# Optimization experiments

Hardware: AMD Instinct MI355X
Metric: run time of the kernel (lower is better)

## Reference

```python
import jax, jax.numpy as jnp
import numpy as np

K = 12          # nsample_k
EPS = 1e-5      # BatchNorm eps


def _init_w(key, shape, fan_in):
    bound = 1.0 / np.sqrt(fan_in)
    return jax.random.uniform(key, shape, jnp.float32, -bound, bound)


def setup_inputs() -> dict:
    key = jax.random.key(0)
    ks = jax.random.split(key, 8)
    B, N = 4, 4096
    p = jax.random.normal(ks[0], (B, N, 3), jnp.float32)
    return {
        "p": p,
        # Conv1d(k=1) weights [out_ch, in_ch]
        "w1": _init_w(ks[1], (18, 36), 36),
        "g1": jnp.ones((18,), jnp.float32), "b1": jnp.zeros((18,), jnp.float32),
        "w2": _init_w(ks[2], (9, 18), 18),
        "g2": jnp.ones((9,), jnp.float32), "b2": jnp.zeros((9,), jnp.float32),
        "w3": _init_w(ks[3], (3, 9), 9),
        "g3": jnp.ones((3,), jnp.float32), "b3": jnp.zeros((3,), jnp.float32),
        "wr": _init_w(ks[4], (1, 3), 3),
        "br": _init_w(ks[5], (1,), 3),
    }


def _bn(x, g, b):
    # BatchNorm1d in training mode over [B, C, L]: stats over (batch, length)
    mu = jnp.mean(x, axis=(0, 2), keepdims=True)
    var = jnp.var(x, axis=(0, 2), keepdims=True)
    return g[None, :, None] * (x - mu) * jax.lax.rsqrt(var + EPS) + b[None, :, None]


def reference(p, w1, g1, b1, w2, g2, b2, w3, g3, b3, wr, br):
    B, N, _ = p.shape
    pf = p.reshape(-1, 3)                                   # [M, 3]
    # KNN over the whole flattened cloud (matches knnquery with a single offset)
    sq = jnp.sum(pf * pf, axis=1)
    d2 = sq[:, None] + sq[None, :] - 2.0 * (pf @ pf.T)       # [M, M]
    _, idx = jax.lax.top_k(-d2, K)                           # K nearest incl. self
    nidx = idx[:, 1:]                                        # drop self -> [M, K-1]
    npos = pf[nidx]                                          # [M, K-1, 3]
    # p_ij = [p_i ; |p_i - p_j|]  -> [M, K, 3] -> [M, K*3]
    pij = jnp.concatenate([pf[:, None, :], jnp.abs(pf[:, None, :] - npos)], axis=1)
    x = pij.reshape(B, N, K * 3).transpose(0, 2, 1)          # [B, 36, N]
    # pointwise MLP: 36 -> 18 -> 9 -> 3, each Conv1x1 + BN + ReLU
    h = jax.nn.relu(_bn(jnp.einsum('oi,bil->bol', w1, x), g1, b1))
    h = jax.nn.relu(_bn(jnp.einsum('oi,bil->bol', w2, h), g2, b2))
    h = jax.nn.relu(_bn(jnp.einsum('oi,bil->bol', w3, h), g3, b3))
    h = h.transpose(0, 2, 1)                                 # [B, N, 3]
    out = h @ wr.T + br                                      # [B, N, 1]
    # F.softmax with no dim on a 3-D tensor -> dim=0 (torch legacy behavior)
    out = jax.nn.softmax(out, axis=0)
    return out.reshape(-1, 1)                                # [B*N, 1]
```

## Files before the change

### kernel.cpp

```cpp
#include <hip/hip_runtime.h>
#include <math.h>

#define NTOT 16384
#define NPT  4096
#define KNN  12
#define NCH  16
#define CHS  (NTOT/NCH)
#define NSMP 128
#define K4   4
#define CAP  32
#define EPSBN 1e-5

#define D_STAT 0
#define D_COEF 60
#define D_Y1   120
#define D_Y2   (D_Y1 + NTOT*18)
#define D_Y3   (D_Y2 + NTOT*9)
#define D_END  (D_Y3 + NTOT*3)

__device__ __forceinline__ float sq_np(float x, float y, float z) {
  return __fadd_rn(__fadd_rn(__fmul_rn(x, x), __fmul_rn(y, y)), __fmul_rn(z, z));
}
__device__ __forceinline__ float d2_np(float sqq, float qx, float qy, float qz,
                                       float sqc, float cx, float cy, float cz) {
  float dot = __fadd_rn(__fadd_rn(__fmul_rn(qx, cx), __fmul_rn(qy, cy)), __fmul_rn(qz, cz));
  return __fsub_rn(__fadd_rn(sqq, sqc), __fmul_rn(2.0f, dot));
}

__global__ __launch_bounds__(256) void k_seed(const float* __restrict__ p,
                                              float* __restrict__ seedd) {
  __shared__ float4 sc[NSMP];
  const int scid = blockIdx.x & (NCH - 1);
  const int qb   = blockIdx.x >> 4;
  const int base = scid * CHS;
  if (threadIdx.x < NSMP) {
    int t = threadIdx.x;
    float x = p[3*(base+t)+0], y = p[3*(base+t)+1], z = p[3*(base+t)+2];
    sc[t] = make_float4(x, y, z, sq_np(x, y, z));
  }
  __syncthreads();
  const int q = qb*256 + (int)threadIdx.x;
  const float qx = p[3*q+0], qy = p[3*q+1], qz = p[3*q+2];
  const float sqq = sq_np(qx, qy, qz);

  float bd[K4];
  #pragma unroll
  for (int k = 0; k < K4; ++k) bd[k] = 3.4e38f;

  for (int j = 0; j < NSMP; ++j) {
    float4 c = sc[j];
    float d2 = d2_np(sqq, qx, qy, qz, c.w, c.x, c.y, c.z);
    if (d2 < bd[K4-1]) {
      #pragma unroll
      for (int k = K4-1; k >= 1; --k) {
        bool m1 = d2 < bd[k-1];
        bool m2 = d2 < bd[k];
        bd[k] = m1 ? bd[k-1] : (m2 ? d2 : bd[k]);
      }
      if (d2 < bd[0]) bd[0] = d2;
    }
  }
  const long o = ((long)q*NCH + scid)*K4;
  #pragma unroll
  for (int k = 0; k < K4; ++k) seedd[o+k] = bd[k];
}

__global__ __launch_bounds__(256) void k_thr(const float* __restrict__ seedd,
                                             float* __restrict__ thr) {
  const int q = blockIdx.x*256 + (int)threadIdx.x;
  float v[NCH*K4];
  #pragma unroll
  for (int i = 0; i < NCH*K4; ++i) v[i] = seedd[(long)q*NCH*K4 + i];
  int sel = 0; float t = 3.4e38f;
  #pragma unroll
  for (int r = 0; r < KNN; ++r) {
    if (sel < KNN) {
      float m = v[0];
      #pragma unroll
      for (int i = 1; i < NCH*K4; ++i) m = fminf(m, v[i]);
      int ce = 0;
      #pragma unroll
      for (int i = 0; i < NCH*K4; ++i) {
        bool e = (v[i] == m);
        ce += e ? 1 : 0;
        v[i] = e ? 3.4e38f : v[i];
      }
      sel += ce; t = m;
    }
  }
  thr[q] = t;
}

__global__ __launch_bounds__(256) void k_main(const float* __restrict__ p,
                                              const float* __restrict__ thr,
                                              unsigned* __restrict__ gcnt,
                                              float* __restrict__ d2f,
                                              unsigned short* __restrict__ gidx) {
  __shared__ float4 mc[CHS];
  const int c  = blockIdx.x & (NCH - 1);
  const int qb = blockIdx.x >> 4;
  const int base = c * CHS;
  for (int t = threadIdx.x; t < CHS; t += 256) {
    float x = p[3*(base+t)+0], y = p[3*(base+t)+1], z = p[3*(base+t)+2];
    mc[t] = make_float4(x, y, z, sq_np(x, y, z));
  }
  __syncthreads();
  const int q = qb*256 + (int)threadIdx.x;
  const float qx = p[3*q+0], qy = p[3*q+1], qz = p[3*q+2];
  const float sqq = sq_np(qx, qy, qz);
  const float tq  = thr[q];

  const long ob = ((long)q*NCH + c)*CAP;
  int cnt = 0;
  for (int j = 0; j < CHS; ++j) {
    float4 cd = mc[j];
    float d2 = d2_np(sqq, qx, qy, qz, cd.w, cd.x, cd.y, cd.z);
    if (d2 <= tq && cnt < CAP) {
      d2f [ob + cnt] = d2;
      gidx[ob + cnt] = (unsigned short)j;
      cnt++;
    }
  }
  gcnt[q*NCH + c] = (unsigned)cnt;
}

__global__ __launch_bounds__(64) void k_l1(const float* __restrict__ p,
                                           const unsigned* __restrict__ gcnt,
                                           const float* __restrict__ d2f,
                                           const unsigned short* __restrict__ gidx,
                                           const float* __restrict__ w1,
                                           double* __restrict__ y1,
                                           double* __restrict__ stat) {
  __shared__ float w1s[18*36];
  for (int t = threadIdx.x; t < 18*36; t += 64) w1s[t] = w1[t];
  __syncthreads();
  const int q = blockIdx.x*64 + (int)threadIdx.x;
  const double dqx = (double)p[3*q+0], dqy = (double)p[3*q+1], dqz = (double)p[3*q+2];

  float bd[KNN]; int bi[KNN];
  #pragma unroll
  for (int k = 0; k < KNN; ++k) { bd[k] = 3.4e38f; bi[k] = 0x7fffffff; }

  for (int c = 0; c < NCH; ++c) {
    int n = (int)gcnt[q*NCH + c]; n = n < CAP ? n : CAP;
    const long ob = ((long)q*NCH + c)*CAP;
    const int gb = c*CHS;
    for (int t = 0; t < n; ++t) {
      float d2 = d2f[ob + t];
      int  idx = gb + (int)gidx[ob + t];
      if (d2 < bd[KNN-1]) {
        #pragma unroll
        for (int k = KNN-1; k >= 1; --k) {
          bool m1 = d2 < bd[k-1];
          bool m2 = d2 < bd[k];
          float nv = m1 ? bd[k-1] : (m2 ? d2  : bd[k]);
          int   ni = m1 ? bi[k-1] : (m2 ? idx : bi[k]);
          bd[k] = nv; bi[k] = ni;
        }
        if (d2 < bd[0]) { bd[0] = d2; bi[0] = idx; }
      }
    }
  }

  double f[36];
  f[0] = dqx; f[1] = dqy; f[2] = dqz;
  #pragma unroll
  for (int r = 0; r < KNN-1; ++r) {
    int j = bi[r+1];
    j = (j < NTOT) ? j : q;
    f[3 + r*3 + 0] = fabs(dqx - (double)p[3*j+0]);
    f[3 + r*3 + 1] = fabs(dqy - (double)p[3*j+1]);
    f[3 + r*3 + 2] = fabs(dqz - (double)p[3*j+2]);
  }

  double v[18];
  #pragma unroll
  for (int o = 0; o < 18; ++o) {
    double s = 0.0;
    #pragma unroll
    for (int i = 0; i < 36; ++i) s += (double)w1s[o*36+i]*f[i];
    v[o] = s;
    y1[(long)q*18 + o] = s;
  }
  #pragma unroll
  for (int o = 0; o < 18; ++o) {
    double s = v[o], ss = v[o]*v[o];
    #pragma unroll
    for (int off = 32; off > 0; off >>= 1) { s += __shfl_down(s, off); ss += __shfl_down(ss, off); }
    if (threadIdx.x == 0) { atomicAdd(&stat[o], s); atomicAdd(&stat[18+o], ss); }
  }
}

__global__ void k_stats(const double* __restrict__ stat, const float* __restrict__ g,
                        const float* __restrict__ bb, double* __restrict__ coef,
                        int C, int sumoff) {
  int c = threadIdx.x;
  if (c < C) {
    const double inv = 1.0/16384.0;
    double mu   = stat[sumoff + c]*inv;
    double va   = stat[sumoff + C + c]*inv - mu*mu;
    double rstd = 1.0/sqrt(va + EPSBN);
    double a    = (double)g[c]*rstd;
    coef[c]     = a;
    coef[C + c] = (double)bb[c] - mu*a;
  }
}

__global__ __launch_bounds__(256) void k_l2(const double* __restrict__ y1,
                                            const float* __restrict__ w2,
                                            const double* __restrict__ coef,
                                            double* __restrict__ y2,
                                            double* __restrict__ stat) {
  const int q = blockIdx.x*256 + (int)threadIdx.x;
  double h[18];
  #pragma unroll
  for (int i = 0; i < 18; ++i) {
    double t = y1[(long)q*18 + i]*coef[i] + coef[18+i];
    h[i] = t > 0.0 ? t : 0.0;
  }
  #pragma unroll
  for (int o = 0; o < 9; ++o) {
    double s = 0.0;
    #pragma unroll
    for (int i = 0; i < 18; ++i) s += (double)w2[o*18+i]*h[i];
    y2[(long)q*9 + o] = s;
    double r1 = s, r2 = s*s;
    #pragma unroll
    for (int off = 32; off > 0; off >>= 1) { r1 += __shfl_down(r1, off); r2 += __shfl_down(r2, off); }
    if ((threadIdx.x & 63) == 0) { atomicAdd(&stat[36+o], r1); atomicAdd(&stat[45+o], r2); }
  }
}

__global__ __launch_bounds__(256) void k_l3(const double* __restrict__ y2,
                                            const float* __restrict__ w3,
                                            const double* __restrict__ coef,
                                            double* __restrict__ y3,
                                            double* __restrict__ stat) {
  const int q = blockIdx.x*256 + (int)threadIdx.x;
  double h[9];
  #pragma unroll
  for (int i = 0; i < 9; ++i) {
    double t = y2[(long)q*9 + i]*coef[i] + coef[9+i];
    h[i] = t > 0.0 ? t : 0.0;
  }
  #pragma unroll
  for (int o = 0; o < 3; ++o) {
    double s = 0.0;
    #pragma unroll
    for (int i = 0; i < 9; ++i) s += (double)w3[o*9+i]*h[i];
    y3[(long)q*3 + o] = s;
    double r1 = s, r2 = s*s;
    #pragma unroll
    for (int off = 32; off > 0; off >>= 1) { r1 += __shfl_down(r1, off); r2 += __shfl_down(r2, off); }
    if ((threadIdx.x & 63) == 0) { atomicAdd(&stat[54+o], r1); atomicAdd(&stat[57+o], r2); }
  }
}

__global__ __launch_bounds__(256) void k_out(const double* __restrict__ y3,
                                             const double* __restrict__ coef3,
                                             const float* __restrict__ wr,
                                             const float* __restrict__ br,
                                             float* __restrict__ out) {
  const int n = blockIdx.x*256 + (int)threadIdx.x;
  if (n >= NPT) return;
  double l[4];
  #pragma unroll
  for (int b = 0; b < 4; ++b) {
    long q = (long)b*NPT + n;
    double h0 = y3[q*3+0]*coef3[0] + coef3[3]; h0 = h0 > 0.0 ? h0 : 0.0;
    double h1 = y3[q*3+1]*coef3[1] + coef3[4]; h1 = h1 > 0.0 ? h1 : 0.0;
    double h2 = y3[q*3+2]*coef3[2] + coef3[5]; h2 = h2 > 0.0 ? h2 : 0.0;
    l[b] = h0*(double)wr[0] + h1*(double)wr[1] + h2*(double)wr[2] + (double)br[0];
  }
  double m = fmax(fmax(l[0], l[1]), fmax(l[2], l[3]));
  double e0 = exp(l[0]-m), e1 = exp(l[1]-m), e2 = exp(l[2]-m), e3 = exp(l[3]-m);
  double inv = 1.0/(e0+e1+e2+e3);
  out[0*NPT+n] = (float)(e0*inv);
  out[1*NPT+n] = (float)(e1*inv);
  out[2*NPT+n] = (float)(e2*inv);
  out[3*NPT+n] = (float)(e3*inv);
}

extern "C" void kernel_launch(void* const* d_in, const int* in_sizes, int n_in,
                              void* d_out, int out_size, void* d_ws, size_t ws_size,
                              hipStream_t stream) {
  const float* p  = (const float*)d_in[0];
  const float* w1 = (const float*)d_in[1];
  const float* g1 = (const float*)d_in[2];
  const float* b1 = (const float*)d_in[3];
  const float* w2 = (const float*)d_in[4];
  const float* g2 = (const float*)d_in[5];
  const float* b2 = (const float*)d_in[6];
  const float* w3 = (const float*)d_in[7];
  const float* g3 = (const float*)d_in[8];
  const float* b3 = (const float*)d_in[9];
  const float* wr = (const float*)d_in[10];
  const float* br = (const float*)d_in[11];

  double* wd   = (double*)d_ws;
  double* stat = wd + D_STAT;
  double* coef = wd + D_COEF;
  double* y1   = wd + D_Y1;
  double* y2   = wd + D_Y2;
  double* y3   = wd + D_Y3;
  float*  fb    = (float*)(wd + D_END);
  float*  seedd = fb;
  float*  thr   = seedd + (long)NTOT*NCH*K4;
  unsigned* gcnt = (unsigned*)(thr + NTOT);
  float*  d2f   = (float*)(gcnt + NTOT*NCH);
  unsigned short* gidx = (unsigned short*)(d2f + (long)NTOT*NCH*CAP);

  hipMemsetAsync(stat, 0, 60*sizeof(double), stream);

  hipLaunchKernelGGL(k_seed, dim3((NTOT/256)*NCH), dim3(256), 0, stream, p, seedd);
  hipLaunchKernelGGL(k_thr,  dim3(NTOT/256), dim3(256), 0, stream, seedd, thr);
  hipLaunchKernelGGL(k_main, dim3((NTOT/256)*NCH), dim3(256), 0, stream, p, thr, gcnt, d2f, gidx);
  hipLaunchKernelGGL(k_l1,   dim3(NTOT/64), dim3(64), 0, stream, p, gcnt, d2f, gidx, w1, y1, stat);
  hipLaunchKernelGGL(k_stats, dim3(1), dim3(32), 0, stream, stat, g1, b1, coef, 18, 0);
  hipLaunchKernelGGL(k_l2,   dim3(NTOT/256), dim3(256), 0, stream, y1, w2, coef, y2, stat);
  hipLaunchKernelGGL(k_stats, dim3(1), dim3(32), 0, stream, stat, g2, b2, coef+36, 9, 36);
  hipLaunchKernelGGL(k_l3,   dim3(NTOT/256), dim3(256), 0, stream, y2, w3, coef+36, y3, stat);
  hipLaunchKernelGGL(k_stats, dim3(1), dim3(32), 0, stream, stat, g3, b3, coef+54, 3, 54);
  hipLaunchKernelGGL(k_out,  dim3(NPT/256), dim3(256), 0, stream, y3, coef+54, wr, br, (float*)d_out);
}
```

Measured before the change: 439.8 us.

## Split KNN selection into a 16-lane cooperative kernel separate from layer-1 features

The fused per-point top-K insertion sort over all 16 chunk candidate lists is replaced by a separate selection kernel. In it, 16 lanes per query each scan their own chunk list and a shuffle-xor argmin picks the global minimum 12 times. A second kernel then builds features from the stored neighbour indices and computes layer 1 with 256-thread blocks. This spreads the serial selection loop across lanes to raise parallelism, at the cost of an extra launch and repeated rescans of each candidate list.

```diff
diff --git a/kernel.cpp b/kernel.cpp
--- a/kernel.cpp
+++ b/kernel.cpp
@@ -124,50 +124,62 @@
   gcnt[q*NCH + c] = (unsigned)cnt;
 }
 
-__global__ __launch_bounds__(64) void k_l1(const float* __restrict__ p,
-                                           const unsigned* __restrict__ gcnt,
-                                           const float* __restrict__ d2f,
-                                           const unsigned short* __restrict__ gidx,
-                                           const float* __restrict__ w1,
-                                           double* __restrict__ y1,
-                                           double* __restrict__ stat) {
+__global__ __launch_bounds__(256) void k_sel(const unsigned* __restrict__ gcnt,
+                                             const float* __restrict__ d2f,
+                                             const unsigned short* __restrict__ gidx,
+                                             int* __restrict__ nbr) {
+  const int grp  = (int)threadIdx.x >> 4;
+  const int lane = (int)threadIdx.x & 15;
+  const int q    = blockIdx.x*16 + grp;
+  const int slot = q*NCH + lane;
+  int n = (int)gcnt[slot]; n = n < CAP ? n : CAP;
+  const long ob = (long)slot*CAP;
+  unsigned consumed = 0;
+
+  #pragma unroll
+  for (int r = 0; r < KNN; ++r) {
+    float mind = 3.4e38f; int tmin = -1;
+    for (int t = 0; t < n; ++t) {
+      float d = d2f[ob + t];
+      bool ok = (((consumed >> t) & 1u) == 0u) && (d < mind);
+      mind = ok ? d : mind;
+      tmin = ok ? t : tmin;
+    }
+    unsigned long long key = 0xFFFFFFFFFFFFFFFFull;
+    if (tmin >= 0) {
+      unsigned u = __float_as_uint(mind);
+      u = (u & 0x80000000u) ? ~u : (u | 0x80000000u);
+      unsigned gi = (unsigned)(lane*CHS) + (unsigned)gidx[ob + tmin];
+      key = ((unsigned long long)u << 32) | gi;
+    }
+    unsigned long long kmin = key;
+    #pragma unroll
+    for (int m = 1; m < 16; m <<= 1) {
+      unsigned long long o = __shfl_xor(kmin, m);
+      kmin = (o < kmin) ? o : kmin;
+    }
+    if (key == kmin && tmin >= 0) consumed |= (1u << tmin);
+    if (lane == 0 && r > 0)
+      nbr[q*(KNN-1) + (r-1)] = (int)(unsigned)(kmin & 0xFFFFFFFFull);
+  }
+}
+
+__global__ __launch_bounds__(256) void k_feat(const float* __restrict__ p,
+                                              const int* __restrict__ nbr,
+                                              const float* __restrict__ w1,
+                                              double* __restrict__ y1,
+                                              double* __restrict__ stat) {
   __shared__ float w1s[18*36];
-  for (int t = threadIdx.x; t < 18*36; t += 64) w1s[t] = w1[t];
+  for (int t = threadIdx.x; t < 18*36; t += 256) w1s[t] = w1[t];
   __syncthreads();
-  const int q = blockIdx.x*64 + (int)threadIdx.x;
+  const int q = blockIdx.x*256 + (int)threadIdx.x;
   const double dqx = (double)p[3*q+0], dqy = (double)p[3*q+1], dqz = (double)p[3*q+2];
-
-  float bd[KNN]; int bi[KNN];
-  #pragma unroll
-  for (int k = 0; k < KNN; ++k) { bd[k] = 3.4e38f; bi[k] = 0x7fffffff; }
-
-  for (int c = 0; c < NCH; ++c) {
-    int n = (int)gcnt[q*NCH + c]; n = n < CAP ? n : CAP;
-    const long ob = ((long)q*NCH + c)*CAP;
-    const int gb = c*CHS;
-    for (int t = 0; t < n; ++t) {
-      float d2 = d2f[ob + t];
-      int  idx = gb + (int)gidx[ob + t];
-      if (d2 < bd[KNN-1]) {
-        #pragma unroll
-        for (int k = KNN-1; k >= 1; --k) {
-          bool m1 = d2 < bd[k-1];
-          bool m2 = d2 < bd[k];
-          float nv = m1 ? bd[k-1] : (m2 ? d2  : bd[k]);
-          int   ni = m1 ? bi[k-1] : (m2 ? idx : bi[k]);
-          bd[k] = nv; bi[k] = ni;
-        }
-        if (d2 < bd[0]) { bd[0] = d2; bi[0] = idx; }
-      }
-    }
-  }
 
   double f[36];
   f[0] = dqx; f[1] = dqy; f[2] = dqz;
   #pragma unroll
   for (int r = 0; r < KNN-1; ++r) {
-    int j = bi[r+1];
-    j = (j < NTOT) ? j : q;
+    int j = nbr[q*(KNN-1) + r];
     f[3 + r*3 + 0] = fabs(dqx - (double)p[3*j+0]);
     f[3 + r*3 + 1] = fabs(dqy - (double)p[3*j+1]);
     f[3 + r*3 + 2] = fabs(dqz - (double)p[3*j+2]);
@@ -187,7 +199,7 @@
     double s = v[o], ss = v[o]*v[o];
     #pragma unroll
     for (int off = 32; off > 0; off >>= 1) { s += __shfl_down(s, off); ss += __shfl_down(ss, off); }
-    if (threadIdx.x == 0) { atomicAdd(&stat[o], s); atomicAdd(&stat[18+o], ss); }
+    if ((threadIdx.x & 63) == 0) { atomicAdd(&stat[o], s); atomicAdd(&stat[18+o], ss); }
   }
 }
 
@@ -309,13 +321,15 @@
   unsigned* gcnt = (unsigned*)(thr + NTOT);
   float*  d2f   = (float*)(gcnt + NTOT*NCH);
   unsigned short* gidx = (unsigned short*)(d2f + (long)NTOT*NCH*CAP);
+  int*    nbr   = (int*)seedd;
 
   hipMemsetAsync(stat, 0, 60*sizeof(double), stream);
 
   hipLaunchKernelGGL(k_seed, dim3((NTOT/256)*NCH), dim3(256), 0, stream, p, seedd);
   hipLaunchKernelGGL(k_thr,  dim3(NTOT/256), dim3(256), 0, stream, seedd, thr);
   hipLaunchKernelGGL(k_main, dim3((NTOT/256)*NCH), dim3(256), 0, stream, p, thr, gcnt, d2f, gidx);
-  hipLaunchKernelGGL(k_l1,   dim3(NTOT/64), dim3(64), 0, stream, p, gcnt, d2f, gidx, w1, y1, stat);
+  hipLaunchKernelGGL(k_sel,  dim3(NTOT/16), dim3(256), 0, stream, gcnt, d2f, gidx, nbr);
+  hipLaunchKernelGGL(k_feat, dim3(NTOT/256), dim3(256), 0, stream, p, nbr, w1, y1, stat);
   hipLaunchKernelGGL(k_stats, dim3(1), dim3(32), 0, stream, stat, g1, b1, coef, 18, 0);
   hipLaunchKernelGGL(k_l2,   dim3(NTOT/256), dim3(256), 0, stream, y1, w2, coef, y2, stat);
   hipLaunchKernelGGL(k_stats, dim3(1), dim3(32), 0, stream, stat, g2, b2, coef+36, 9, 36);
```

Result: faster. 427.5 us (-2.8%).
